# Performance work log

Hardware: AMD Instinct MI355X
Metric: run time of the kernel (lower is better)

Reference implementation:

```python
import jax, jax.numpy as jnp
import numpy as np

B, V, T = 1, 1, 2
C = 128          # in_features
H = 4            # num_heads
NKV = 12288      # cells at cross zoom 5 (12*4**5)
S = NKV          # query groups == cross cells
NH = 9           # neighborhood size (cell + 8 ring)
NPQ = 16         # queries per group: 4**(7-5)
NQ = S * NPQ     # cells at zoom 7


def _ln(x, scale, bias, eps=1e-5):
    mu = jnp.mean(x, axis=-1, keepdims=True)
    var = jnp.mean(jnp.square(x - mu), axis=-1, keepdims=True)
    return (x - mu) * jax.lax.rsqrt(var + eps) * scale + bias


def setup_inputs() -> dict:
    key = jax.random.key(0)
    ks = jax.random.split(key, 12)
    w = lambda k, shp: jax.random.normal(k, shp, jnp.float32) * (1.0 / np.sqrt(shp[0]))
    return {
        "x_q":  jax.random.normal(ks[0], (B, V, T, NQ, C), jnp.float32),
        "x_kv": jax.random.normal(ks[1], (B, V, T, NKV, C), jnp.float32),
        "nh_idx":  jax.random.randint(ks[2], (S, NH), 0, NKV, jnp.int32),
        "nh_mask": jnp.ones((S, NH), jnp.bool_),
        "ln_q_s": jnp.ones((C,), jnp.float32), "ln_q_b": jnp.zeros((C,), jnp.float32),
        "Wq": w(ks[3], (C, C)), "bq": jnp.zeros((C,), jnp.float32),
        "ln_kv_s": jnp.ones((C,), jnp.float32), "ln_kv_b": jnp.zeros((C,), jnp.float32),
        "Wkv": w(ks[4], (C, 2 * C)), "bkv": jnp.zeros((2 * C,), jnp.float32),
        "Wa_q": w(ks[5], (C, C)),
        "W_out": w(ks[6], (C, C)), "b_out": jnp.zeros((C,), jnp.float32),
        "gamma": jnp.full((C,), 1e-6, jnp.float32),
        "ln_m_s": jnp.ones((C,), jnp.float32), "ln_m_b": jnp.zeros((C,), jnp.float32),
        "Wm": w(ks[7], (C, C)), "bm": jnp.zeros((C,), jnp.float32),
        "W1": w(ks[8], (C, C)), "b1": jnp.zeros((C,), jnp.float32),
        "W2": w(ks[9], (C, C)), "b2": jnp.zeros((C,), jnp.float32),
        "gamma_mlp": jnp.full((C,), 1e-6, jnp.float32),
    }


def reference(x_q, x_kv, nh_idx, nh_mask, ln_q_s, ln_q_b, Wq, bq,
              ln_kv_s, ln_kv_b, Wkv, bkv, Wa_q, W_out, b_out, gamma,
              ln_m_s, ln_m_b, Wm, bm, W1, b1, W2, b2, gamma_mlp):
    hd = C // H
    # q_layer: LN + Linear
    q = _ln(x_q, ln_q_s, ln_q_b) @ Wq + bq                      # [B,V,T,NQ,C]
    # kv_layer: LN + Linear to 2C (K|V)
    kv = _ln(x_kv, ln_kv_s, ln_kv_b) @ Wkv + bkv                # [B,V,T,NKV,2C]
    # grid neighborhood gather (get_nh)
    kv_nh = kv[:, :, :, nh_idx, :]                              # [B,V,T,S,NH,2C]
    k, vv = jnp.split(kv_nh, 2, axis=-1)                        # [B,V,T,S,NH,C] each
    # group queries per cross cell
    q = q.reshape(B, V, T, S, NPQ, C)
    # cross attention (q projected inside attention; k/v pre-projected)
    qh = (q @ Wa_q).reshape(B, V, T, S, NPQ, H, hd)
    kh = k.reshape(B, V, T, S, NH, H, hd)
    vh = vv.reshape(B, V, T, S, NH, H, hd)
    scores = jnp.einsum('bvtsqhd,bvtsnhd->bvtshqn', qh, kh) / np.sqrt(hd)
    bias = jnp.where(nh_mask, 0.0, -1e9).astype(scores.dtype)   # mask==False -> masked
    scores = scores + bias[None, None, None, :, None, None, :]
    attn = jax.nn.softmax(scores, axis=-1)
    out = jnp.einsum('bvtshqn,bvtsnhd->bvtsqhd', attn, vh).reshape(B, V, T, S, NPQ, C)
    out = out @ W_out + b_out
    x = x_q + gamma * out.reshape(B, V, T, NQ, C)
    # gated MLP residual
    h = _ln(x, ln_m_s, ln_m_b) @ Wm + bm
    m = jax.nn.gelu(h @ W1 + b1) @ W2 + b2
    x = x + gamma_mlp * m
    return x
```

## Files before the change

### kernel.cpp

```cpp
#include <hip/hip_runtime.h>
#include <hip/hip_bf16.h>

#define DEVINL __device__ __forceinline__

typedef __attribute__((ext_vector_type(8))) short bf16x8;
typedef __attribute__((ext_vector_type(4))) float f32x4;

static constexpr int C   = 128;
static constexpr int SS  = 12288;
static constexpr int NPQ = 16;

DEVINL f32x4 mfma16(bf16x8 a, bf16x8 b, f32x4 c) {
  return __builtin_amdgcn_mfma_f32_16x16x32_bf16(a, b, c, 0, 0, 0);
}
DEVINL f32x4 f32x4_zero() { f32x4 z; z[0] = 0.f; z[1] = 0.f; z[2] = 0.f; z[3] = 0.f; return z; }

DEVINL unsigned short f2bf(float f) {
  __hip_bfloat16 h = __float2bfloat16(f);
  return __builtin_bit_cast(unsigned short, h);
}
DEVINL float bf2f(unsigned short u) {
  unsigned int v = ((unsigned int)u) << 16;
  return __builtin_bit_cast(float, v);
}
DEVINL unsigned cvt_pk_bf16(float lo_, float hi_) {
  unsigned r;
  asm volatile("v_cvt_pk_bf16_f32 %0, %1, %2" : "=v"(r) : "v"(lo_), "v"(hi_));
  return r;
}
DEVINL int swz(int r, int c) {
  return (r << 7) + ((((c >> 3) ^ (r & 7))) << 3) + (c & 7);
}
DEVINL void wave_sync() {
  asm volatile("s_waitcnt lgkmcnt(0)" ::: "memory");
  __builtin_amdgcn_sched_barrier(0);
}
DEVINL float gelu_f(float x) {
  float u = 0.7978845608028654f * (x + 0.044715f * x * x * x);
  float t = 1.0f - 2.0f / (__expf(2.0f * u) + 1.0f);
  return 0.5f * x * (1.0f + t);
}

DEVINL void stage_half(const unsigned short* __restrict__ wf_all,
                       unsigned short* Wslot, int half, int tid) {
  const unsigned short* src = wf_all + (size_t)half * 8192;
  const int wv = tid >> 6, l = tid & 63;
#pragma unroll
  for (int r = 0; r < 4; ++r) {
    int off = (r * 4 + wv) * 512;
    __builtin_amdgcn_global_load_lds(
        (const __attribute__((address_space(1))) unsigned int*)(src + off + l * 8),
        (__attribute__((address_space(3))) unsigned int*)(Wslot + off),
        16, 0, 0);
  }
}

__global__ void prep_weights(const float* __restrict__ w0, const float* __restrict__ w1,
                             const float* __restrict__ w2, const float* __restrict__ w3,
                             const float* __restrict__ w4, const float* __restrict__ w5,
                             unsigned short* __restrict__ wfrag) {
  int gid = blockIdx.x * 256 + threadIdx.x;
  int widx = gid >> 14, f = gid & 16383;
  const float* W = (widx == 0) ? w0 : (widx == 1) ? w1 : (widx == 2) ? w2
                 : (widx == 3) ? w3 : (widx == 4) ? w4 : w5;
  int i = f & 7, l = (f >> 3) & 63, nt = (f >> 9) & 7, kt = f >> 12;
  int k = kt * 32 + (l >> 4) * 8 + i;
  int n = nt * 16 + (l & 15);
  wfrag[gid] = f2bf(W[k * 128 + n]);
}

__global__ __launch_bounds__(256) void kv_proj(
    const float* __restrict__ xkv, const float* __restrict__ lns,
    const float* __restrict__ lnb, const float* __restrict__ Wkv,
    const float* __restrict__ bkv, unsigned short* __restrict__ kvout) {
  __shared__ float y[16][132];
  const int tid = threadIdx.x;
  const size_t rb = (size_t)blockIdx.x * 16;

  {
    int r = tid >> 4, p = tid & 15;
    const float* xr = xkv + (rb + r) * C + p * 8;
    float v[8];
    float sum = 0.f, sq = 0.f;
#pragma unroll
    for (int i = 0; i < 2; ++i) {
      float4 q4 = *(const float4*)(xr + i * 4);
      v[i * 4 + 0] = q4.x; v[i * 4 + 1] = q4.y; v[i * 4 + 2] = q4.z; v[i * 4 + 3] = q4.w;
      sum += q4.x + q4.y + q4.z + q4.w;
      sq  += q4.x * q4.x + q4.y * q4.y + q4.z * q4.z + q4.w * q4.w;
    }
    sum += __shfl_xor(sum, 1, 16); sum += __shfl_xor(sum, 2, 16);
    sum += __shfl_xor(sum, 4, 16); sum += __shfl_xor(sum, 8, 16);
    sq  += __shfl_xor(sq, 1, 16);  sq  += __shfl_xor(sq, 2, 16);
    sq  += __shfl_xor(sq, 4, 16);  sq  += __shfl_xor(sq, 8, 16);
    float mu = sum * (1.0f / 128.f);
    float rs = rsqrtf(sq * (1.0f / 128.f) - mu * mu + 1e-5f);
#pragma unroll
    for (int i = 0; i < 8; ++i) {
      int c = p * 8 + i;
      y[r][c] = (v[i] - mu) * rs * lns[c] + lnb[c];
    }
  }
  __syncthreads();

  const int c2 = tid;
  float acc[16];
#pragma unroll
  for (int r = 0; r < 16; ++r) acc[r] = 0.f;
  for (int c = 0; c < 128; c += 4) {
    float w0 = Wkv[(c + 0) * 256 + c2];
    float w1 = Wkv[(c + 1) * 256 + c2];
    float w2 = Wkv[(c + 2) * 256 + c2];
    float w3 = Wkv[(c + 3) * 256 + c2];
#pragma unroll
    for (int r = 0; r < 16; ++r) {
      float4 yv = *(const float4*)&y[r][c];
      acc[r] += yv.x * w0 + yv.y * w1 + yv.z * w2 + yv.w * w3;
    }
  }
  float bb = bkv[c2];
#pragma unroll
  for (int r = 0; r < 16; ++r)
    kvout[(rb + r) * 256 + c2] = f2bf(acc[r] + bb);
}

template <int MODE>
DEVINL void mm16(const unsigned short* src, unsigned short* dst,
                 unsigned short (*Wb)[8192],
                 const unsigned short* __restrict__ wf_all, int j0,
                 const float* __restrict__ bias,
                 const float* __restrict__ xqw, const float* __restrict__ gamma,
                 const unsigned short* xK, const float* __restrict__ gmlp,
                 float* __restrict__ outw, int tid) {
  const int l = tid & 63, lo = l & 15, g = l >> 4;
  f32x4 acc[8];
#pragma unroll
  for (int nt = 0; nt < 8; ++nt) acc[nt] = f32x4_zero();

#pragma unroll
  for (int hh = 0; hh < 2; ++hh) {
    const int j = j0 + hh;
    if (j + 1 < 12) stage_half(wf_all, Wb[(j + 1) & 1], j + 1, tid);
    const unsigned short* W = Wb[j & 1];
#pragma unroll
    for (int k2 = 0; k2 < 2; ++k2) {
      int kt = hh * 2 + k2;
      bf16x8 a = *(const bf16x8*)(src + swz(lo, kt * 32 + g * 8));
#pragma unroll
      for (int nt = 0; nt < 8; ++nt) {
        bf16x8 b = *(const bf16x8*)(W + (k2 * 8 + nt) * 512 + l * 8);
        acc[nt] = mfma16(a, b, acc[nt]);
      }
    }
    __syncthreads();
  }

#pragma unroll
  for (int nt = 0; nt < 8; ++nt) {
    int col = nt * 16 + lo;
    float bv = (MODE == 4) ? 0.0f : bias[col];
    float gm = (MODE == 2) ? gamma[col] : 0.0f;
    float gp = (MODE == 3) ? gmlp[col] : 0.0f;
#pragma unroll
    for (int e = 0; e < 4; ++e) {
      int row = g * 4 + e;
      float v = acc[nt][e] + bv;
      if (MODE == 1) v = gelu_f(v);
      if (MODE == 4) v = acc[nt][e] * 0.17677669529663687f;
      if (MODE == 2) v = xqw[row * C + col] + gm * v;
      if (MODE == 3) {
        float x2 = bf2f(xK[swz(row, col)]);
        outw[row * C + col] = x2 + gp * v;
      } else {
        dst[swz(row, col)] = f2bf(v);
      }
    }
  }
}

__global__ __launch_bounds__(256, 2) void fused_main(
    const float* __restrict__ xq, const int* __restrict__ nh_idx,
    const unsigned char* __restrict__ nh_mask,
    const unsigned short* __restrict__ wfrag,
    const unsigned short* __restrict__ kvws,
    const float* __restrict__ ln_q_s, const float* __restrict__ ln_q_b,
    const float* __restrict__ bq, const float* __restrict__ b_out,
    const float* __restrict__ gamma, const float* __restrict__ ln_m_s,
    const float* __restrict__ ln_m_b, const float* __restrict__ bm,
    const float* __restrict__ b1, const float* __restrict__ b2,
    const float* __restrict__ gmlp, float* __restrict__ out) {
  __shared__ __align__(16) unsigned short Wb[2][8192];
  __shared__ __align__(16) unsigned short SU[4][5248];

  const int tid = threadIdx.x, l = tid & 63, wv = tid >> 6;
  const int lo = l & 15, g = l >> 4;
  const int bid = blockIdx.x;
  const int t = bid / (SS / 4);
  const int s = (bid % (SS / 4)) * 4 + wv;
  const float* xqw = xq + (size_t)(t * SS + s) * NPQ * C;
  float* outw = out + (size_t)(t * SS + s) * NPQ * C;
  unsigned short* X  = SU[wv];
  unsigned short* K  = SU[wv] + 2048;
  unsigned short* VT = SU[wv] + 3200;

  stage_half(wfrag, Wb[0], 0, tid);
  float sbias[4];
#pragma unroll
  for (int e = 0; e < 4; ++e) {
    int n = g * 4 + e;
    sbias[e] = (n < 9) ? (nh_mask[s * 9 + n] ? 0.0f : -1e9f) : -1e9f;
  }
  uint4 gr[5];
  {
    int ch = l & 31;
#pragma unroll
    for (int i = 0; i < 5; ++i) {
      int idx = i * 64 + l;
      if (idx < 288) {
        int n = i * 2 + (l >> 5);
        int jrow = nh_idx[s * 9 + n];
        gr[i] = *(const uint4*)(kvws + ((size_t)(t * SS + jrow)) * 256 + ch * 8);
      }
    }
  }
  {
    uint4 z; z.x = 0u; z.y = 0u; z.z = 0u; z.w = 0u;
#pragma unroll
    for (int r = 0; r < 4; ++r)
      *(uint4*)(VT + (r * 64 + l) * 8) = z;
  }
  wave_sync();

  {
    int r = l >> 2, p = l & 3;
    const float* xr = xqw + r * C + p * 32;
    float v[32];
    float sum = 0.f, sq = 0.f;
#pragma unroll
    for (int i = 0; i < 8; ++i) {
      float4 q4 = *(const float4*)(xr + i * 4);
      v[i * 4 + 0] = q4.x; v[i * 4 + 1] = q4.y; v[i * 4 + 2] = q4.z; v[i * 4 + 3] = q4.w;
      sum += q4.x + q4.y + q4.z + q4.w;
      sq  += q4.x * q4.x + q4.y * q4.y + q4.z * q4.z + q4.w * q4.w;
    }
    sum += __shfl_xor(sum, 1, 4); sum += __shfl_xor(sum, 2, 4);
    sq  += __shfl_xor(sq, 1, 4);  sq  += __shfl_xor(sq, 2, 4);
    float mu = sum * (1.0f / C);
    float rs = rsqrtf(sq * (1.0f / C) - mu * mu + 1e-5f);
#pragma unroll
    for (int cc = 0; cc < 4; ++cc) {
      unsigned short pk[8];
#pragma unroll
      for (int i = 0; i < 8; ++i) {
        int c = p * 32 + cc * 8 + i;
        pk[i] = f2bf((v[cc * 8 + i] - mu) * rs * ln_q_s[c] + ln_q_b[c]);
      }
      *(uint4*)&X[swz(r, p * 32 + cc * 8)] = *(const uint4*)pk;
    }
  }
  {
    int ch = l & 31;
#pragma unroll
    for (int i = 0; i < 5; ++i) {
      int idx = i * 64 + l;
      if (idx < 288) {
        int n = i * 2 + (l >> 5);
        if (ch < 16) {
          *(uint4*)(K + n * 128 + ((ch ^ (n & 7)) << 3)) = gr[i];
        } else {
          int d0 = (ch - 16) * 8;
          int nt = d0 >> 4;
          int base = nt * 256 + (n >> 1) * 32 + (d0 & 15) * 2 + (n & 1);
          const unsigned short* u = (const unsigned short*)&gr[i];
#pragma unroll
          for (int dd = 0; dd < 8; ++dd) VT[base + dd * 2] = u[dd];
        }
      }
    }
  }
  wave_sync();
  __syncthreads();

  mm16<0>(X, X, Wb, wfrag, 0, bq, nullptr, nullptr, nullptr, nullptr, nullptr, tid);
  wave_sync();
  mm16<4>(X, X, Wb, wfrag, 2, nullptr, nullptr, nullptr, nullptr, nullptr, nullptr, tid);
  wave_sync();

  {
    const int krow = (lo > 8) ? 8 : lo;
    f32x4 st[4];
#pragma unroll
    for (int h = 0; h < 4; ++h) {
      bf16x8 ka = *(const bf16x8*)(K + swz(krow, h * 32 + g * 8));
      bf16x8 qb = *(const bf16x8*)(X + swz(lo,   h * 32 + g * 8));
      st[h] = mfma16(ka, qb, f32x4_zero());
    }
    bf16x8 pfrag[4];
#pragma unroll
    for (int h = 0; h < 4; ++h) {
      float p0 = st[h][0] + sbias[0], p1 = st[h][1] + sbias[1];
      float p2 = st[h][2] + sbias[2], p3 = st[h][3] + sbias[3];
      float m = fmaxf(fmaxf(p0, p1), fmaxf(p2, p3));
      m = fmaxf(m, __shfl_xor(m, 16));
      m = fmaxf(m, __shfl_xor(m, 32));
      p0 = __expf(p0 - m); p1 = __expf(p1 - m);
      p2 = __expf(p2 - m); p3 = __expf(p3 - m);
      float ss = p0 + p1 + p2 + p3;
      ss += __shfl_xor(ss, 16);
      ss += __shfl_xor(ss, 32);
      float inv = 1.0f / ss;
      p0 *= inv; p1 *= inv; p2 *= inv; p3 *= inv;
      float b0 = __shfl_xor(p0, 16), b1 = __shfl_xor(p1, 16),
            b2 = __shfl_xor(p2, 16), b3 = __shfl_xor(p3, 16);
      float c0 = __shfl_xor(p0, 32), c1 = __shfl_xor(p1, 32),
            c2 = __shfl_xor(p2, 32), c3 = __shfl_xor(p3, 32);
      float d0 = __shfl_xor(p0, 48), d1 = __shfl_xor(p1, 48),
            d2 = __shfl_xor(p2, 48), d3 = __shfl_xor(p3, 48);
      float L0 = (g == 0) ? p0 : (g == 1) ? d0 : 0.f;
      float L1 = (g == 0) ? p1 : (g == 1) ? d1 : 0.f;
      float L2 = (g == 0) ? p2 : (g == 1) ? d2 : 0.f;
      float L3 = (g == 0) ? p3 : (g == 1) ? d3 : 0.f;
      float H0 = (g == 0) ? b0 : (g == 1) ? c0 : 0.f;
      float H1 = (g == 0) ? b1 : (g == 1) ? c1 : 0.f;
      float H2 = (g == 0) ? b2 : (g == 1) ? c2 : 0.f;
      float H3 = (g == 0) ? b3 : (g == 1) ? c3 : 0.f;
      unsigned dw0 = cvt_pk_bf16(L0, L1), dw1 = cvt_pk_bf16(L2, L3);
      unsigned dw2 = cvt_pk_bf16(H0, H1), dw3 = cvt_pk_bf16(H2, H3);
      uint4 pu; pu.x = dw0; pu.y = dw1; pu.z = dw2; pu.w = dw3;
      pfrag[h] = __builtin_bit_cast(bf16x8, pu);
    }
    f32x4 oacc[8];
#pragma unroll
    for (int nt = 0; nt < 8; ++nt) {
      unsigned vw0 = 0, vw1 = 0, vw2 = 0, vw3 = 0;
      if (g < 2) {
        const unsigned short* vb = VT + nt * 256 + g * 128 + lo * 2;
        vw0 = *(const unsigned*)(vb);
        vw1 = *(const unsigned*)(vb + 32);
        vw2 = *(const unsigned*)(vb + 64);
        vw3 = *(const unsigned*)(vb + 96);
      }
      uint4 vu; vu.x = vw0; vu.y = vw1; vu.z = vw2; vu.w = vw3;
      bf16x8 vfrag = __builtin_bit_cast(bf16x8, vu);
      oacc[nt] = mfma16(pfrag[nt >> 1], vfrag, f32x4_zero());
    }
    wave_sync();
#pragma unroll
    for (int nt = 0; nt < 8; ++nt)
#pragma unroll
      for (int e = 0; e < 4; ++e)
        X[swz(g * 4 + e, nt * 16 + lo)] = f2bf(oacc[nt][e]);
  }
  wave_sync();

  mm16<2>(X, VT, Wb, wfrag, 4, b_out, xqw, gamma, nullptr, nullptr, nullptr, tid);
  wave_sync();

  {
    int r = l >> 2, p = l & 3;
    float v[32];
    float sum = 0.f, sq = 0.f;
#pragma unroll
    for (int cc = 0; cc < 4; ++cc) {
      uint4 u = *(const uint4*)(VT + swz(r, p * 32 + cc * 8));
      const unsigned short* up = (const unsigned short*)&u;
#pragma unroll
      for (int i = 0; i < 8; ++i) {
        float xv = bf2f(up[i]);
        v[cc * 8 + i] = xv;
        sum += xv; sq += xv * xv;
      }
    }
    sum += __shfl_xor(sum, 1, 4); sum += __shfl_xor(sum, 2, 4);
    sq  += __shfl_xor(sq, 1, 4);  sq  += __shfl_xor(sq, 2, 4);
    float mu = sum * (1.0f / C);
    float rs = rsqrtf(sq * (1.0f / C) - mu * mu + 1e-5f);
#pragma unroll
    for (int cc = 0; cc < 4; ++cc) {
      unsigned short pk[8];
#pragma unroll
      for (int i = 0; i < 8; ++i) {
        int c = p * 32 + cc * 8 + i;
        pk[i] = f2bf((v[cc * 8 + i] - mu) * rs * ln_m_s[c] + ln_m_b[c]);
      }
      *(uint4*)&X[swz(r, p * 32 + cc * 8)] = *(const uint4*)pk;
    }
  }
  wave_sync();

  mm16<0>(X, X, Wb, wfrag, 6, bm, nullptr, nullptr, nullptr, nullptr, nullptr, tid);
  wave_sync();
  mm16<1>(X, X, Wb, wfrag, 8, b1, nullptr, nullptr, nullptr, nullptr, nullptr, tid);
  wave_sync();
  mm16<3>(X, nullptr, Wb, wfrag, 10, b2, nullptr, nullptr, VT, gmlp, outw, tid);
}

extern "C" void kernel_launch(void* const* d_in, const int* in_sizes, int n_in,
                              void* d_out, int out_size, void* d_ws, size_t ws_size,
                              hipStream_t stream) {
  const float* x_q     = (const float*)d_in[0];
  const float* x_kv    = (const float*)d_in[1];
  const int* nh_idx    = (const int*)d_in[2];
  const unsigned char* nh_mask = (const unsigned char*)d_in[3];
  const float* ln_q_s  = (const float*)d_in[4];
  const float* ln_q_b  = (const float*)d_in[5];
  const float* Wq      = (const float*)d_in[6];
  const float* bq      = (const float*)d_in[7];
  const float* ln_kv_s = (const float*)d_in[8];
  const float* ln_kv_b = (const float*)d_in[9];
  const float* Wkv     = (const float*)d_in[10];
  const float* bkv     = (const float*)d_in[11];
  const float* Wa_q    = (const float*)d_in[12];
  const float* W_out   = (const float*)d_in[13];
  const float* b_out   = (const float*)d_in[14];
  const float* gamma   = (const float*)d_in[15];
  const float* ln_m_s  = (const float*)d_in[16];
  const float* ln_m_b  = (const float*)d_in[17];
  const float* Wm      = (const float*)d_in[18];
  const float* bm      = (const float*)d_in[19];
  const float* W1      = (const float*)d_in[20];
  const float* b1      = (const float*)d_in[21];
  const float* W2      = (const float*)d_in[22];
  const float* b2      = (const float*)d_in[23];
  const float* gmlp    = (const float*)d_in[24];

  unsigned short* wfrag = (unsigned short*)d_ws;
  unsigned short* kvws  = wfrag + 6 * 16384;

  prep_weights<<<384, 256, 0, stream>>>(Wq, Wa_q, W_out, Wm, W1, W2, wfrag);
  kv_proj<<<1536, 256, 0, stream>>>(x_kv, ln_kv_s, ln_kv_b, Wkv, bkv, kvws);
  fused_main<<<6144, 256, 0, stream>>>(x_q, nh_idx, nh_mask, wfrag, kvws,
                                       ln_q_s, ln_q_b, bq, b_out, gamma,
                                       ln_m_s, ln_m_b, bm, b1, b2, gmlp,
                                       (float*)d_out);
}
```

Measured before the change: 379.0 us.

## Flip GEMM orientation, keep residual in registers, shrink LDS for higher occupancy

The per-wave 16-row GEMMs now use weights as the A operand and activations as B, so each lane holds four contiguous output columns. This enables vectorized bias, residual and LayerNorm epilogues with packed bf16 stores, and the post-attention residual is kept in registers instead of an LDS buffer. Weight staging drops to quarter-matrix slices, the V transpose reuses the X buffer, and the Wa_q scale is folded into the weights at prep time. Together these cut shared memory so occupancy can rise from 2 to 3 blocks per CU. The cost is more barrier rounds per GEMM and higher register pressure from the 16-entry residual array.

```diff
diff --git a/kernel.cpp b/kernel.cpp
--- a/kernel.cpp
+++ b/kernel.cpp
@@ -6,21 +6,19 @@
 typedef __attribute__((ext_vector_type(8))) short bf16x8;
 typedef __attribute__((ext_vector_type(4))) float f32x4;
 
-static constexpr int C   = 128;
-static constexpr int SS  = 12288;
-static constexpr int NPQ = 16;
-
+static constexpr int SS = 12288;
+static constexpr float QKS = 0.17677669529663687f;
+
+DEVINL f32x4 f32x4_zero() { f32x4 z; z[0]=0.f; z[1]=0.f; z[2]=0.f; z[3]=0.f; return z; }
 DEVINL f32x4 mfma16(bf16x8 a, bf16x8 b, f32x4 c) {
   return __builtin_amdgcn_mfma_f32_16x16x32_bf16(a, b, c, 0, 0, 0);
 }
-DEVINL f32x4 f32x4_zero() { f32x4 z; z[0] = 0.f; z[1] = 0.f; z[2] = 0.f; z[3] = 0.f; return z; }
-
 DEVINL unsigned short f2bf(float f) {
   __hip_bfloat16 h = __float2bfloat16(f);
   return __builtin_bit_cast(unsigned short, h);
 }
 DEVINL float bf2f(unsigned short u) {
-  unsigned int v = ((unsigned int)u) << 16;
+  unsigned v = ((unsigned)u) << 16;
   return __builtin_bit_cast(float, v);
 }
 DEVINL unsigned cvt_pk_bf16(float lo_, float hi_) {
@@ -41,17 +39,16 @@
   return 0.5f * x * (1.0f + t);
 }
 
-DEVINL void stage_half(const unsigned short* __restrict__ wf_all,
-                       unsigned short* Wslot, int half, int tid) {
-  const unsigned short* src = wf_all + (size_t)half * 8192;
+DEVINL void stage8(const unsigned short* __restrict__ wf_all,
+                   unsigned short* slot, int slice, int tid) {
+  const unsigned short* src = wf_all + (size_t)slice * 4096;
   const int wv = tid >> 6, l = tid & 63;
 #pragma unroll
-  for (int r = 0; r < 4; ++r) {
+  for (int r = 0; r < 2; ++r) {
     int off = (r * 4 + wv) * 512;
     __builtin_amdgcn_global_load_lds(
         (const __attribute__((address_space(1))) unsigned int*)(src + off + l * 8),
-        (__attribute__((address_space(3))) unsigned int*)(Wslot + off),
-        16, 0, 0);
+        (__attribute__((address_space(3))) unsigned int*)(slot + off), 16, 0, 0);
   }
 }
 
@@ -60,13 +57,18 @@
                              const float* __restrict__ w4, const float* __restrict__ w5,
                              unsigned short* __restrict__ wfrag) {
   int gid = blockIdx.x * 256 + threadIdx.x;
-  int widx = gid >> 14, f = gid & 16383;
-  const float* W = (widx == 0) ? w0 : (widx == 1) ? w1 : (widx == 2) ? w2
-                 : (widx == 3) ? w3 : (widx == 4) ? w4 : w5;
-  int i = f & 7, l = (f >> 3) & 63, nt = (f >> 9) & 7, kt = f >> 12;
+  int i  = gid & 7;
+  int l  = (gid >> 3) & 63;
+  int mt = (gid >> 9) & 7;
+  int kt = (gid >> 12) & 3;
+  int mat = gid >> 14;
+  const float* W = (mat == 0) ? w0 : (mat == 1) ? w1 : (mat == 2) ? w2
+                 : (mat == 3) ? w3 : (mat == 4) ? w4 : w5;
   int k = kt * 32 + (l >> 4) * 8 + i;
-  int n = nt * 16 + (l & 15);
-  wfrag[gid] = f2bf(W[k * 128 + n]);
+  int c = mt * 16 + (l & 15);
+  float v = W[k * 128 + c];
+  if (mat == 1) v *= QKS;
+  wfrag[gid] = f2bf(v);
 }
 
 __global__ __launch_bounds__(256) void kv_proj(
@@ -76,25 +78,24 @@
   __shared__ float y[16][132];
   const int tid = threadIdx.x;
   const size_t rb = (size_t)blockIdx.x * 16;
-
   {
     int r = tid >> 4, p = tid & 15;
-    const float* xr = xkv + (rb + r) * C + p * 8;
+    const float* xr = xkv + (rb + r) * 128 + p * 8;
     float v[8];
     float sum = 0.f, sq = 0.f;
 #pragma unroll
     for (int i = 0; i < 2; ++i) {
       float4 q4 = *(const float4*)(xr + i * 4);
-      v[i * 4 + 0] = q4.x; v[i * 4 + 1] = q4.y; v[i * 4 + 2] = q4.z; v[i * 4 + 3] = q4.w;
+      v[i*4+0]=q4.x; v[i*4+1]=q4.y; v[i*4+2]=q4.z; v[i*4+3]=q4.w;
       sum += q4.x + q4.y + q4.z + q4.w;
-      sq  += q4.x * q4.x + q4.y * q4.y + q4.z * q4.z + q4.w * q4.w;
+      sq  += q4.x*q4.x + q4.y*q4.y + q4.z*q4.z + q4.w*q4.w;
     }
     sum += __shfl_xor(sum, 1, 16); sum += __shfl_xor(sum, 2, 16);
     sum += __shfl_xor(sum, 4, 16); sum += __shfl_xor(sum, 8, 16);
     sq  += __shfl_xor(sq, 1, 16);  sq  += __shfl_xor(sq, 2, 16);
     sq  += __shfl_xor(sq, 4, 16);  sq  += __shfl_xor(sq, 8, 16);
-    float mu = sum * (1.0f / 128.f);
-    float rs = rsqrtf(sq * (1.0f / 128.f) - mu * mu + 1e-5f);
+    float mu = sum * (1.0f/128.f);
+    float rs = rsqrtf(sq * (1.0f/128.f) - mu*mu + 1e-5f);
 #pragma unroll
     for (int i = 0; i < 8; ++i) {
       int c = p * 8 + i;
@@ -102,20 +103,19 @@
     }
   }
   __syncthreads();
-
   const int c2 = tid;
   float acc[16];
 #pragma unroll
   for (int r = 0; r < 16; ++r) acc[r] = 0.f;
   for (int c = 0; c < 128; c += 4) {
-    float w0 = Wkv[(c + 0) * 256 + c2];
-    float w1 = Wkv[(c + 1) * 256 + c2];
-    float w2 = Wkv[(c + 2) * 256 + c2];
-    float w3 = Wkv[(c + 3) * 256 + c2];
+    float w0 = Wkv[(c+0)*256 + c2];
+    float w1 = Wkv[(c+1)*256 + c2];
+    float w2 = Wkv[(c+2)*256 + c2];
+    float w3 = Wkv[(c+3)*256 + c2];
 #pragma unroll
     for (int r = 0; r < 16; ++r) {
       float4 yv = *(const float4*)&y[r][c];
-      acc[r] += yv.x * w0 + yv.y * w1 + yv.z * w2 + yv.w * w3;
+      acc[r] += yv.x*w0 + yv.y*w1 + yv.z*w2 + yv.w*w3;
     }
   }
   float bb = bkv[c2];
@@ -125,60 +125,66 @@
 }
 
 template <int MODE>
-DEVINL void mm16(const unsigned short* src, unsigned short* dst,
-                 unsigned short (*Wb)[8192],
-                 const unsigned short* __restrict__ wf_all, int j0,
-                 const float* __restrict__ bias,
-                 const float* __restrict__ xqw, const float* __restrict__ gamma,
-                 const unsigned short* xK, const float* __restrict__ gmlp,
-                 float* __restrict__ outw, int tid) {
+DEVINL void mmFlip(unsigned short* X, unsigned short (*Wb)[4096],
+                   const unsigned short* __restrict__ wf_all, int j0,
+                   const float* __restrict__ bias,
+                   const float* __restrict__ xqw, const float* __restrict__ gamma,
+                   unsigned* x2p, const float* __restrict__ gmlp,
+                   float* __restrict__ outw, int tid) {
   const int l = tid & 63, lo = l & 15, g = l >> 4;
   f32x4 acc[8];
 #pragma unroll
-  for (int nt = 0; nt < 8; ++nt) acc[nt] = f32x4_zero();
-
-#pragma unroll
-  for (int hh = 0; hh < 2; ++hh) {
-    const int j = j0 + hh;
-    if (j + 1 < 12) stage_half(wf_all, Wb[(j + 1) & 1], j + 1, tid);
+  for (int mt = 0; mt < 8; ++mt) acc[mt] = f32x4_zero();
+
+#pragma unroll
+  for (int kt = 0; kt < 4; ++kt) {
+    const int j = j0 + kt;
+    if (j + 1 < 24) stage8(wf_all, Wb[(j + 1) & 1], j + 1, tid);
     const unsigned short* W = Wb[j & 1];
-#pragma unroll
-    for (int k2 = 0; k2 < 2; ++k2) {
-      int kt = hh * 2 + k2;
-      bf16x8 a = *(const bf16x8*)(src + swz(lo, kt * 32 + g * 8));
-#pragma unroll
-      for (int nt = 0; nt < 8; ++nt) {
-        bf16x8 b = *(const bf16x8*)(W + (k2 * 8 + nt) * 512 + l * 8);
-        acc[nt] = mfma16(a, b, acc[nt]);
-      }
+    bf16x8 b = *(const bf16x8*)(X + swz(lo, kt * 32 + g * 8));
+#pragma unroll
+    for (int mt = 0; mt < 8; ++mt) {
+      bf16x8 a = *(const bf16x8*)(W + (mt * 64 + l) * 8);
+      acc[mt] = mfma16(a, b, acc[mt]);
     }
     __syncthreads();
   }
 
 #pragma unroll
-  for (int nt = 0; nt < 8; ++nt) {
-    int col = nt * 16 + lo;
-    float bv = (MODE == 4) ? 0.0f : bias[col];
-    float gm = (MODE == 2) ? gamma[col] : 0.0f;
-    float gp = (MODE == 3) ? gmlp[col] : 0.0f;
-#pragma unroll
-    for (int e = 0; e < 4; ++e) {
-      int row = g * 4 + e;
-      float v = acc[nt][e] + bv;
-      if (MODE == 1) v = gelu_f(v);
-      if (MODE == 4) v = acc[nt][e] * 0.17677669529663687f;
-      if (MODE == 2) v = xqw[row * C + col] + gm * v;
-      if (MODE == 3) {
-        float x2 = bf2f(xK[swz(row, col)]);
-        outw[row * C + col] = x2 + gp * v;
-      } else {
-        dst[swz(row, col)] = f2bf(v);
-      }
-    }
-  }
-}
-
-__global__ __launch_bounds__(256, 2) void fused_main(
+  for (int mt = 0; mt < 8; ++mt) {
+    int c0 = mt * 16 + g * 4;
+    float v0 = acc[mt][0], v1 = acc[mt][1], v2 = acc[mt][2], v3 = acc[mt][3];
+    if (bias) {
+      float4 b4 = *(const float4*)(bias + c0);
+      v0 += b4.x; v1 += b4.y; v2 += b4.z; v3 += b4.w;
+    }
+    if (MODE == 1) { v0 = gelu_f(v0); v1 = gelu_f(v1); v2 = gelu_f(v2); v3 = gelu_f(v3); }
+    if (MODE == 2) {
+      float4 x4 = *(const float4*)(xqw + lo * 128 + c0);
+      float4 g4 = *(const float4*)(gamma + c0);
+      v0 = x4.x + g4.x * v0; v1 = x4.y + g4.y * v1;
+      v2 = x4.z + g4.z * v2; v3 = x4.w + g4.w * v3;
+      x2p[2 * mt]     = cvt_pk_bf16(v0, v1);
+      x2p[2 * mt + 1] = cvt_pk_bf16(v2, v3);
+    } else if (MODE == 3) {
+      float4 p4 = *(const float4*)(gmlp + c0);
+      unsigned xa = x2p[2 * mt], xb = x2p[2 * mt + 1];
+      float4 o;
+      o.x = bf2f((unsigned short)(xa & 0xffff))  + p4.x * v0;
+      o.y = bf2f((unsigned short)(xa >> 16))     + p4.y * v1;
+      o.z = bf2f((unsigned short)(xb & 0xffff))  + p4.z * v2;
+      o.w = bf2f((unsigned short)(xb >> 16))     + p4.w * v3;
+      *(float4*)(outw + lo * 128 + c0) = o;
+    } else {
+      uint2 w2;
+      w2.x = cvt_pk_bf16(v0, v1);
+      w2.y = cvt_pk_bf16(v2, v3);
+      *(uint2*)(X + swz(lo, c0)) = w2;
+    }
+  }
+}
+
+__global__ __launch_bounds__(256, 3) void fused_main(
     const float* __restrict__ xq, const int* __restrict__ nh_idx,
     const unsigned char* __restrict__ nh_mask,
     const unsigned short* __restrict__ wfrag,
@@ -189,21 +195,19 @@
     const float* __restrict__ ln_m_b, const float* __restrict__ bm,
     const float* __restrict__ b1, const float* __restrict__ b2,
     const float* __restrict__ gmlp, float* __restrict__ out) {
-  __shared__ __align__(16) unsigned short Wb[2][8192];
-  __shared__ __align__(16) unsigned short SU[4][5248];
+  __shared__ __align__(16) unsigned short Wb[2][4096];
+  __shared__ __align__(16) unsigned short SU[4][3200];
 
   const int tid = threadIdx.x, l = tid & 63, wv = tid >> 6;
   const int lo = l & 15, g = l >> 4;
-  const int bid = blockIdx.x;
-  const int t = bid / (SS / 4);
-  const int s = (bid % (SS / 4)) * 4 + wv;
-  const float* xqw = xq + (size_t)(t * SS + s) * NPQ * C;
-  float* outw = out + (size_t)(t * SS + s) * NPQ * C;
-  unsigned short* X  = SU[wv];
-  unsigned short* K  = SU[wv] + 2048;
-  unsigned short* VT = SU[wv] + 3200;
-
-  stage_half(wfrag, Wb[0], 0, tid);
+  const int su = blockIdx.x * 4 + wv;
+  const int t = su / SS, s = su - t * SS;
+  const float* xqw = xq + (size_t)su * 2048;
+  float* outw = out + (size_t)su * 2048;
+  unsigned short* X = SU[wv];
+  unsigned short* K = SU[wv] + 2048;
+
+  stage8(wfrag, Wb[0], 0, tid);
   float sbias[4];
 #pragma unroll
   for (int e = 0; e < 4; ++e) {
@@ -212,78 +216,59 @@
   }
   uint4 gr[5];
   {
-    int ch = l & 31;
 #pragma unroll
     for (int i = 0; i < 5; ++i) {
       int idx = i * 64 + l;
       if (idx < 288) {
-        int n = i * 2 + (l >> 5);
+        int n = idx >> 5, ch = idx & 31;
         int jrow = nh_idx[s * 9 + n];
         gr[i] = *(const uint4*)(kvws + ((size_t)(t * SS + jrow)) * 256 + ch * 8);
       }
     }
-  }
-  {
-    uint4 z; z.x = 0u; z.y = 0u; z.z = 0u; z.w = 0u;
-#pragma unroll
-    for (int r = 0; r < 4; ++r)
-      *(uint4*)(VT + (r * 64 + l) * 8) = z;
-  }
-  wave_sync();
-
-  {
-    int r = l >> 2, p = l & 3;
-    const float* xr = xqw + r * C + p * 32;
-    float v[32];
-    float sum = 0.f, sq = 0.f;
-#pragma unroll
-    for (int i = 0; i < 8; ++i) {
-      float4 q4 = *(const float4*)(xr + i * 4);
-      v[i * 4 + 0] = q4.x; v[i * 4 + 1] = q4.y; v[i * 4 + 2] = q4.z; v[i * 4 + 3] = q4.w;
-      sum += q4.x + q4.y + q4.z + q4.w;
-      sq  += q4.x * q4.x + q4.y * q4.y + q4.z * q4.z + q4.w * q4.w;
-    }
-    sum += __shfl_xor(sum, 1, 4); sum += __shfl_xor(sum, 2, 4);
-    sq  += __shfl_xor(sq, 1, 4);  sq  += __shfl_xor(sq, 2, 4);
-    float mu = sum * (1.0f / C);
-    float rs = rsqrtf(sq * (1.0f / C) - mu * mu + 1e-5f);
-#pragma unroll
-    for (int cc = 0; cc < 4; ++cc) {
-      unsigned short pk[8];
-#pragma unroll
-      for (int i = 0; i < 8; ++i) {
-        int c = p * 32 + cc * 8 + i;
-        pk[i] = f2bf((v[cc * 8 + i] - mu) * rs * ln_q_s[c] + ln_q_b[c]);
-      }
-      *(uint4*)&X[swz(r, p * 32 + cc * 8)] = *(const uint4*)pk;
-    }
-  }
-  {
-    int ch = l & 31;
 #pragma unroll
     for (int i = 0; i < 5; ++i) {
       int idx = i * 64 + l;
-      if (idx < 288) {
-        int n = i * 2 + (l >> 5);
-        if (ch < 16) {
-          *(uint4*)(K + n * 128 + ((ch ^ (n & 7)) << 3)) = gr[i];
-        } else {
-          int d0 = (ch - 16) * 8;
-          int nt = d0 >> 4;
-          int base = nt * 256 + (n >> 1) * 32 + (d0 & 15) * 2 + (n & 1);
-          const unsigned short* u = (const unsigned short*)&gr[i];
-#pragma unroll
-          for (int dd = 0; dd < 8; ++dd) VT[base + dd * 2] = u[dd];
-        }
+      if (idx < 288 && (idx & 31) < 16) {
+        int n = idx >> 5, ch = idx & 31;
+        *(uint4*)(K + n * 128 + ((ch ^ (n & 7)) << 3)) = gr[i];
       }
     }
   }
+
+  {
+    float4 xv[8];
+    float sum = 0.f, sq = 0.f;
+#pragma unroll
+    for (int mt = 0; mt < 8; ++mt) {
+      xv[mt] = *(const float4*)(xqw + lo * 128 + mt * 16 + g * 4);
+      sum += xv[mt].x + xv[mt].y + xv[mt].z + xv[mt].w;
+      sq  += xv[mt].x*xv[mt].x + xv[mt].y*xv[mt].y + xv[mt].z*xv[mt].z + xv[mt].w*xv[mt].w;
+    }
+    sum += __shfl_xor(sum, 16); sum += __shfl_xor(sum, 32);
+    sq  += __shfl_xor(sq, 16);  sq  += __shfl_xor(sq, 32);
+    float mu = sum * (1.0f/128.f);
+    float rs = rsqrtf(sq * (1.0f/128.f) - mu*mu + 1e-5f);
+#pragma unroll
+    for (int mt = 0; mt < 8; ++mt) {
+      int c0 = mt * 16 + g * 4;
+      float4 s4 = *(const float4*)(ln_q_s + c0);
+      float4 b4 = *(const float4*)(ln_q_b + c0);
+      uint2 w2;
+      w2.x = cvt_pk_bf16((xv[mt].x - mu) * rs * s4.x + b4.x,
+                         (xv[mt].y - mu) * rs * s4.y + b4.y);
+      w2.y = cvt_pk_bf16((xv[mt].z - mu) * rs * s4.z + b4.z,
+                         (xv[mt].w - mu) * rs * s4.w + b4.w);
+      *(uint2*)(X + swz(lo, c0)) = w2;
+    }
+  }
   wave_sync();
   __syncthreads();
 
-  mm16<0>(X, X, Wb, wfrag, 0, bq, nullptr, nullptr, nullptr, nullptr, nullptr, tid);
-  wave_sync();
-  mm16<4>(X, X, Wb, wfrag, 2, nullptr, nullptr, nullptr, nullptr, nullptr, nullptr, tid);
+  unsigned x2p[16];
+
+  mmFlip<0>(X, Wb, wfrag, 0, bq, nullptr, nullptr, nullptr, nullptr, nullptr, tid);
+  wave_sync();
+  mmFlip<0>(X, Wb, wfrag, 4, nullptr, nullptr, nullptr, nullptr, nullptr, nullptr, tid);
   wave_sync();
 
   {
@@ -295,46 +280,58 @@
       bf16x8 qb = *(const bf16x8*)(X + swz(lo,   h * 32 + g * 8));
       st[h] = mfma16(ka, qb, f32x4_zero());
     }
+    wave_sync();
+#pragma unroll
+    for (int i = 0; i < 5; ++i) {
+      int idx = i * 64 + l;
+      if (idx < 288 && (idx & 31) >= 16) {
+        int n = idx >> 5, d0 = ((idx & 31) - 16) * 8;
+        int nt = d0 >> 4;
+        int base = nt * 256 + (n >> 1) * 32 + (d0 & 15) * 2 + (n & 1);
+        const unsigned short* u = (const unsigned short*)&gr[i];
+#pragma unroll
+        for (int dd = 0; dd < 8; ++dd) X[base + dd * 2] = u[dd];
+      }
+    }
     bf16x8 pfrag[4];
 #pragma unroll
     for (int h = 0; h < 4; ++h) {
       float p0 = st[h][0] + sbias[0], p1 = st[h][1] + sbias[1];
       float p2 = st[h][2] + sbias[2], p3 = st[h][3] + sbias[3];
       float m = fmaxf(fmaxf(p0, p1), fmaxf(p2, p3));
-      m = fmaxf(m, __shfl_xor(m, 16));
-      m = fmaxf(m, __shfl_xor(m, 32));
+      m = fmaxf(m, __shfl_xor(m, 16)); m = fmaxf(m, __shfl_xor(m, 32));
       p0 = __expf(p0 - m); p1 = __expf(p1 - m);
       p2 = __expf(p2 - m); p3 = __expf(p3 - m);
       float ss = p0 + p1 + p2 + p3;
-      ss += __shfl_xor(ss, 16);
-      ss += __shfl_xor(ss, 32);
+      ss += __shfl_xor(ss, 16); ss += __shfl_xor(ss, 32);
       float inv = 1.0f / ss;
       p0 *= inv; p1 *= inv; p2 *= inv; p3 *= inv;
       float b0 = __shfl_xor(p0, 16), b1 = __shfl_xor(p1, 16),
-            b2 = __shfl_xor(p2, 16), b3 = __shfl_xor(p3, 16);
-      float c0 = __shfl_xor(p0, 32), c1 = __shfl_xor(p1, 32),
+            b2_ = __shfl_xor(p2, 16), b3 = __shfl_xor(p3, 16);
+      float c0_ = __shfl_xor(p0, 32), c1 = __shfl_xor(p1, 32),
             c2 = __shfl_xor(p2, 32), c3 = __shfl_xor(p3, 32);
-      float d0 = __shfl_xor(p0, 48), d1 = __shfl_xor(p1, 48),
+      float d0_ = __shfl_xor(p0, 48), d1 = __shfl_xor(p1, 48),
             d2 = __shfl_xor(p2, 48), d3 = __shfl_xor(p3, 48);
-      float L0 = (g == 0) ? p0 : (g == 1) ? d0 : 0.f;
+      float L0 = (g == 0) ? p0 : (g == 1) ? d0_ : 0.f;
       float L1 = (g == 0) ? p1 : (g == 1) ? d1 : 0.f;
       float L2 = (g == 0) ? p2 : (g == 1) ? d2 : 0.f;
       float L3 = (g == 0) ? p3 : (g == 1) ? d3 : 0.f;
-      float H0 = (g == 0) ? b0 : (g == 1) ? c0 : 0.f;
+      float H0 = (g == 0) ? b0 : (g == 1) ? c0_ : 0.f;
       float H1 = (g == 0) ? b1 : (g == 1) ? c1 : 0.f;
-      float H2 = (g == 0) ? b2 : (g == 1) ? c2 : 0.f;
+      float H2 = (g == 0) ? b2_ : (g == 1) ? c2 : 0.f;
       float H3 = (g == 0) ? b3 : (g == 1) ? c3 : 0.f;
-      unsigned dw0 = cvt_pk_bf16(L0, L1), dw1 = cvt_pk_bf16(L2, L3);
-      unsigned dw2 = cvt_pk_bf16(H0, H1), dw3 = cvt_pk_bf16(H2, H3);
-      uint4 pu; pu.x = dw0; pu.y = dw1; pu.z = dw2; pu.w = dw3;
+      uint4 pu;
+      pu.x = cvt_pk_bf16(L0, L1); pu.y = cvt_pk_bf16(L2, L3);
+      pu.z = cvt_pk_bf16(H0, H1); pu.w = cvt_pk_bf16(H2, H3);
       pfrag[h] = __builtin_bit_cast(bf16x8, pu);
     }
+    wave_sync();
     f32x4 oacc[8];
 #pragma unroll
     for (int nt = 0; nt < 8; ++nt) {
       unsigned vw0 = 0, vw1 = 0, vw2 = 0, vw3 = 0;
       if (g < 2) {
-        const unsigned short* vb = VT + nt * 256 + g * 128 + lo * 2;
+        const unsigned short* vb = X + nt * 256 + g * 128 + lo * 2;
         vw0 = *(const unsigned*)(vb);
         vw1 = *(const unsigned*)(vb + 32);
         vw2 = *(const unsigned*)(vb + 64);
@@ -349,50 +346,50 @@
     for (int nt = 0; nt < 8; ++nt)
 #pragma unroll
       for (int e = 0; e < 4; ++e)
-        X[swz(g * 4 + e, nt * 16 + lo)] = f2bf(oacc[nt][e]);
-  }
-  wave_sync();
-
-  mm16<2>(X, VT, Wb, wfrag, 4, b_out, xqw, gamma, nullptr, nullptr, nullptr, tid);
-  wave_sync();
+        X[swz(g * 4 + e, nt * 16 + lo)] = (unsigned short)(cvt_pk_bf16(oacc[nt][e], 0.f) & 0xffff);
+    wave_sync();
+  }
+
+  mmFlip<2>(X, Wb, wfrag, 8, b_out, xqw, gamma, x2p, nullptr, nullptr, tid);
 
   {
-    int r = l >> 2, p = l & 3;
-    float v[32];
     float sum = 0.f, sq = 0.f;
-#pragma unroll
-    for (int cc = 0; cc < 4; ++cc) {
-      uint4 u = *(const uint4*)(VT + swz(r, p * 32 + cc * 8));
-      const unsigned short* up = (const unsigned short*)&u;
-#pragma unroll
-      for (int i = 0; i < 8; ++i) {
-        float xv = bf2f(up[i]);
-        v[cc * 8 + i] = xv;
-        sum += xv; sq += xv * xv;
-      }
-    }
-    sum += __shfl_xor(sum, 1, 4); sum += __shfl_xor(sum, 2, 4);
-    sq  += __shfl_xor(sq, 1, 4);  sq  += __shfl_xor(sq, 2, 4);
-    float mu = sum * (1.0f / C);
-    float rs = rsqrtf(sq * (1.0f / C) - mu * mu + 1e-5f);
-#pragma unroll
-    for (int cc = 0; cc < 4; ++cc) {
-      unsigned short pk[8];
-#pragma unroll
-      for (int i = 0; i < 8; ++i) {
-        int c = p * 32 + cc * 8 + i;
-        pk[i] = f2bf((v[cc * 8 + i] - mu) * rs * ln_m_s[c] + ln_m_b[c]);
-      }
-      *(uint4*)&X[swz(r, p * 32 + cc * 8)] = *(const uint4*)pk;
-    }
-  }
-  wave_sync();
-
-  mm16<0>(X, X, Wb, wfrag, 6, bm, nullptr, nullptr, nullptr, nullptr, nullptr, tid);
-  wave_sync();
-  mm16<1>(X, X, Wb, wfrag, 8, b1, nullptr, nullptr, nullptr, nullptr, nullptr, tid);
-  wave_sync();
-  mm16<3>(X, nullptr, Wb, wfrag, 10, b2, nullptr, nullptr, VT, gmlp, outw, tid);
+    float xv[4];
+#pragma unroll
+    for (int mt = 0; mt < 8; ++mt) {
+      unsigned xa = x2p[2*mt], xb = x2p[2*mt+1];
+      xv[0] = bf2f((unsigned short)(xa & 0xffff));
+      xv[1] = bf2f((unsigned short)(xa >> 16));
+      xv[2] = bf2f((unsigned short)(xb & 0xffff));
+      xv[3] = bf2f((unsigned short)(xb >> 16));
+      sum += xv[0] + xv[1] + xv[2] + xv[3];
+      sq  += xv[0]*xv[0] + xv[1]*xv[1] + xv[2]*xv[2] + xv[3]*xv[3];
+    }
+    sum += __shfl_xor(sum, 16); sum += __shfl_xor(sum, 32);
+    sq  += __shfl_xor(sq, 16);  sq  += __shfl_xor(sq, 32);
+    float mu = sum * (1.0f/128.f);
+    float rs = rsqrtf(sq * (1.0f/128.f) - mu*mu + 1e-5f);
+#pragma unroll
+    for (int mt = 0; mt < 8; ++mt) {
+      int c0 = mt * 16 + g * 4;
+      unsigned xa = x2p[2*mt], xb = x2p[2*mt+1];
+      float4 s4 = *(const float4*)(ln_m_s + c0);
+      float4 b4 = *(const float4*)(ln_m_b + c0);
+      uint2 w2;
+      w2.x = cvt_pk_bf16((bf2f((unsigned short)(xa & 0xffff)) - mu) * rs * s4.x + b4.x,
+                         (bf2f((unsigned short)(xa >> 16))    - mu) * rs * s4.y + b4.y);
+      w2.y = cvt_pk_bf16((bf2f((unsigned short)(xb & 0xffff)) - mu) * rs * s4.z + b4.z,
+                         (bf2f((unsigned short)(xb >> 16))    - mu) * rs * s4.w + b4.w);
+      *(uint2*)(X + swz(lo, c0)) = w2;
+    }
+  }
+  wave_sync();
+
+  mmFlip<0>(X, Wb, wfrag, 12, bm, nullptr, nullptr, nullptr, nullptr, nullptr, tid);
+  wave_sync();
+  mmFlip<1>(X, Wb, wfrag, 16, b1, nullptr, nullptr, nullptr, nullptr, nullptr, tid);
+  wave_sync();
+  mmFlip<3>(X, Wb, wfrag, 20, b2, nullptr, nullptr, x2p, gmlp, outw, tid);
 }
 
 extern "C" void kernel_launch(void* const* d_in, const int* in_sizes, int n_in,
@@ -429,8 +426,7 @@
 
   prep_weights<<<384, 256, 0, stream>>>(Wq, Wa_q, W_out, Wm, W1, W2, wfrag);
   kv_proj<<<1536, 256, 0, stream>>>(x_kv, ln_kv_s, ln_kv_b, Wkv, bkv, kvws);
-  fused_main<<<6144, 256, 0, stream>>>(x_q, nh_idx, nh_mask, wfrag, kvws,
-                                       ln_q_s, ln_q_b, bq, b_out, gamma,
-                                       ln_m_s, ln_m_b, bm, b1, b2, gmlp,
-                                       (float*)d_out);
-}
+  fused_main<<<6144, 256, 0, stream>>>(
+      x_q, nh_idx, nh_mask, wfrag, kvws, ln_q_s, ln_q_b, bq, b_out, gamma,
+      ln_m_s, ln_m_b, bm, b1, b2, gmlp, (float*)d_out);
+}
```

New measurement: 345.3 us. 1.1x faster.
